# Optimization experiments

Hardware: AMD Instinct MI355X
Metric: run time of the kernel (lower is better)

The kernel has to match this reference:

```python
import jax, jax.numpy as jnp
import numpy as np


def _pairwise_iou(boxes):
    # boxes: [B, N, 4] in (x1, y1, x2, y2); returns IoU [B, N, N]
    area = (boxes[..., 2] - boxes[..., 0]) * (boxes[..., 3] - boxes[..., 1])  # [B, N]
    lt = jnp.maximum(boxes[:, :, None, :2], boxes[:, None, :, :2])  # [B, N, N, 2]
    rb = jnp.minimum(boxes[:, :, None, 2:], boxes[:, None, :, 2:])
    wh = jnp.clip(rb - lt, 0.0)
    inter = wh[..., 0] * wh[..., 1]  # [B, N, N]
    union = area[:, :, None] + area[:, None, :] - inter
    return inter / jnp.maximum(union, 1e-6)


def setup_inputs() -> dict:
    key = jax.random.key(0)
    kxy, kwh, ks = jax.random.split(key, 3)
    B, N, C = 4, 2048, 4
    xy = jax.random.uniform(kxy, (B, N, 2), dtype=jnp.float32) * 1000.0
    wh = jax.random.uniform(kwh, (B, N, 2), dtype=jnp.float32) * 100.0 + 1.0
    boxes = jnp.concatenate([xy, xy + wh], axis=-1)  # valid xyxy boxes
    scores = jax.random.uniform(ks, (B, C, N), dtype=jnp.float32)
    return {
        "boxes": boxes,
        "scores": scores,
        "iou_threshold": jnp.array([0.5], dtype=jnp.float32),
        "score_threshold": jnp.array([0.05], dtype=jnp.float32),
    }


def reference(boxes, scores, iou_threshold, score_threshold):
    # Greedy NMS-match (mmcv.ops.nms_match semantics), per batch and class.
    # Returns match: [B, C, N] int32 where match[b,c,n] is the index of the
    # group-leader (kept) box that box n belongs to, or -1 if unmatched
    # (i.e. score <= score_threshold).
    B, N, _ = boxes.shape
    C = scores.shape[1]
    thr = iou_threshold[0]
    sthr = score_threshold[0]

    iou = _pairwise_iou(boxes)  # [B, N, N] (shared across classes)
    order = jnp.argsort(-scores, axis=-1)  # [B, C, N], score-descending

    suppressed0 = scores <= sthr            # boxes below score threshold never match
    match0 = jnp.full((B, C, N), -1, jnp.int32)
    b_idx = jnp.arange(B)[:, None]          # [B, 1] for per-batch IoU row gather

    def step(carry, cand):
        # cand: [B, C] box index with next-highest score in each (batch, class)
        suppressed, match = carry           # [B, C, N] bool / int32
        cand_sup = jnp.take_along_axis(suppressed, cand[..., None], axis=-1)[..., 0]
        active = ~cand_sup                  # [B, C]: candidate not yet grouped
        cand_iou = iou[b_idx, cand]         # [B, C, N] IoU of candidate vs all boxes
        matched = active[..., None] & (~suppressed) & (cand_iou > thr)
        match = jnp.where(matched, cand[..., None].astype(jnp.int32), match)
        return (suppressed | matched, match), None

    xs = jnp.moveaxis(order, -1, 0)         # [N, B, C]: sequential greedy order
    (_, match), _ = jax.lax.scan(step, (suppressed0, match0), xs)
    return match
```

## Files before the change

kernel.cpp:

```cpp
#include <hip/hip_runtime.h>
#include <stdint.h>

#define N_   2048
#define NW   64
#define CLS  4
#define B_   4
#define ORD_STRIDE (N_ + 64)

__global__ __launch_bounds__(256) void mask_or_sort(
    const float4* __restrict__ boxes, const float* __restrict__ thr_p,
    const float* __restrict__ scores, const float* __restrict__ sthr_p,
    uint32_t* __restrict__ ov, int* __restrict__ order,
    int* __restrict__ rk, uint32_t* __restrict__ sup0ws)
{
  __shared__ __align__(16) unsigned char lds_raw[32768];
  __shared__ uint32_t sup_l[NW];
  __shared__ int cnt_s;

  if (blockIdx.x < 256) {
    float4* sb = (float4*)lds_raw;
    const int b    = blockIdx.x >> 6;
    const int tile = blockIdx.x & 63;
    const float thr = thr_p[0];
    for (int i = threadIdx.x; i < N_; i += 256) sb[i] = boxes[b * N_ + i];
    __syncthreads();
    const int wv = threadIdx.x >> 6;
    const int ln = threadIdx.x & 63;
    const int r0 = tile * 32 + wv * 8;
    float4 bi[8]; float areai[8];
    #pragma unroll
    for (int rr = 0; rr < 8; ++rr) {
      bi[rr] = sb[r0 + rr];
      areai[rr] = (bi[rr].z - bi[rr].x) * (bi[rr].w - bi[rr].y);
    }
    uint32_t myw[8] = {0, 0, 0, 0, 0, 0, 0, 0};
    for (int g = 0; g < 32; ++g) {
      const float4 bj = sb[g * 64 + ln];
      const float areaj = (bj.z - bj.x) * (bj.w - bj.y);
      const bool sel = ((ln >> 1) == g);
      const bool hi  = (ln & 1);
      #pragma unroll
      for (int rr = 0; rr < 8; ++rr) {
        const float xx1 = fmaxf(bi[rr].x, bj.x);
        const float yy1 = fmaxf(bi[rr].y, bj.y);
        const float xx2 = fminf(bi[rr].z, bj.z);
        const float yy2 = fminf(bi[rr].w, bj.w);
        const float iw = fmaxf(xx2 - xx1, 0.0f);
        const float ih = fmaxf(yy2 - yy1, 0.0f);
        const float inter = iw * ih;
        const float uni = fmaxf(areai[rr] + areaj - inter, 1e-6f);
        const unsigned long long bal = __ballot(inter / uni > thr);
        const uint32_t w = hi ? (uint32_t)(bal >> 32) : (uint32_t)bal;
        if (sel) myw[rr] = w;
      }
    }
    #pragma unroll
    for (int rr = 0; rr < 8; ++rr)
      ov[((size_t)(b * N_ + r0 + rr)) * NW + ln] = myw[rr];
  } else {
    unsigned long long* sp = (unsigned long long*)lds_raw;
    const int bc = blockIdx.x - 256;
    const float sthr = sthr_p[0];
    const float* s = scores + (size_t)bc * N_;
    for (int i = threadIdx.x; i < N_; i += 256) {
      const float v = s[i];
      uint32_t u = __float_as_uint(v);
      u = (u >> 31) ? ~u : (u | 0x80000000u);
      sp[i] = ((unsigned long long)u << 32) | (uint32_t)(~(uint32_t)i);
      const unsigned long long bal = __ballot(v <= sthr);
      if ((threadIdx.x & 63) == 0) {
        sup_l[(i >> 5)]     = (uint32_t)bal;
        sup_l[(i >> 5) + 1] = (uint32_t)(bal >> 32);
      }
    }
    for (int size = 2; size <= N_; size <<= 1) {
      for (int stride = size >> 1; stride > 0; stride >>= 1) {
        __syncthreads();
        for (int t = threadIdx.x; t < N_ / 2; t += 256) {
          const int pos = 2 * t - (t & (stride - 1));
          const bool desc = ((t & (size >> 1)) == 0);
          const unsigned long long a = sp[pos], c = sp[pos + stride];
          if (desc != (a > c)) { sp[pos] = c; sp[pos + stride] = a; }
        }
      }
    }
    __syncthreads();
    if (threadIdx.x == 0) {
      int c2 = 0;
      for (int w = 0; w < NW; ++w) c2 += __popc(sup_l[w]);
      cnt_s = N_ - c2;
    }
    __syncthreads();
    const int cnt = cnt_s;
    const int last = (cnt > 0) ? (int)~(uint32_t)sp[cnt - 1] : 0;
    int* ord_o = order + (size_t)bc * ORD_STRIDE;
    int* rk_o  = rk    + (size_t)bc * N_;
    for (int i = threadIdx.x; i < N_; i += 256) {
      const int idx = (int)~(uint32_t)sp[i];
      ord_o[i] = (i < cnt || cnt == 0) ? idx : last;
      rk_o[idx] = i;
    }
    for (int i = N_ + threadIdx.x; i < ORD_STRIDE; i += 256) ord_o[i] = last;
    if (threadIdx.x < NW) sup0ws[bc * NW + threadIdx.x] = sup_l[threadIdx.x];
  }
}


#define S6_(rw,bt) \
  "v_and_b32 v35, v" #rw ", v34\n\t"           \
  "v_cmp_ne_u32 vcc, 0, v35\n\t"               \
  "s_cmp_lg_u64 vcc, 0\n\t"                    \
  "s_cselect_b32 s40, 0, -1\n\t"               \
  "v_and_b32 v37, s40, v" #bt "\n\t"           \
  "v_or_b32 v34, v34, v37\n\t"

#define RF_(rw,st) \
  "v_lshlrev_b32 v38, 8, v" #st "\n\t"         \
  "v_add_u32 v38, v38, v33\n\t"                \
  "global_load_dword v" #rw ", v38, %[B]\n\t"

#define MB_(bt,st) \
  "v_bfe_u32 v36, v" #st ", 5, 6\n\t"          \
  "v_cmp_eq_u32 s[42:43], v36, v32\n\t"        \
  "v_cndmask_b32 v37, 0, v40, s[42:43]\n\t"    \
  "v_lshlrev_b32 v" #bt ", v" #st ", v37\n\t"

#define CAND(rw,bt,st) S6_(rw,bt) RF_(rw,st) MB_(bt,st)
#define CP(rw,bt,st)   RF_(rw,st) MB_(bt,st)

#define DSR4 \
  "ds_read_b128 v[140:143], v39\n\t"           \
  "ds_read_b128 v[144:147], v39 offset:16\n\t" \
  "ds_read_b128 v[148:151], v39 offset:32\n\t" \
  "ds_read_b128 v[152:155], v39 offset:48\n\t" \
  "v_add_u32 v39, 64, v39\n\t"

#define PH_HDR "s_waitcnt vmcnt(32)\n\t" "s_waitcnt lgkmcnt(0)\n\t"

#define PH_A PH_HDR \
  CAND(92,44,140)  CAND(93,45,141)  CAND(94,46,142)  CAND(95,47,143)  \
  CAND(96,48,144)  CAND(97,49,145)  CAND(98,50,146)  CAND(99,51,147)  \
  CAND(100,52,148) CAND(101,53,149) CAND(102,54,150) CAND(103,55,151) \
  CAND(104,56,152) CAND(105,57,153) CAND(106,58,154) CAND(107,59,155) DSR4
#define PH_B PH_HDR \
  CAND(108,60,140) CAND(109,61,141) CAND(110,62,142) CAND(111,63,143) \
  CAND(112,64,144) CAND(113,65,145) CAND(114,66,146) CAND(115,67,147) \
  CAND(116,68,148) CAND(117,69,149) CAND(118,70,150) CAND(119,71,151) \
  CAND(120,72,152) CAND(121,73,153) CAND(122,74,154) CAND(123,75,155) DSR4
#define PH_C PH_HDR \
  CAND(124,76,140) CAND(125,77,141) CAND(126,78,142) CAND(127,79,143) \
  CAND(128,80,144) CAND(129,81,145) CAND(130,82,146) CAND(131,83,147) \
  CAND(132,84,148) CAND(133,85,149) CAND(134,86,150) CAND(135,87,151) \
  CAND(136,88,152) CAND(137,89,153) CAND(138,90,154) CAND(139,91,155) DSR4

#define PRO_A \
  CP(92,44,140)  CP(93,45,141)  CP(94,46,142)  CP(95,47,143)  \
  CP(96,48,144)  CP(97,49,145)  CP(98,50,146)  CP(99,51,147)  \
  CP(100,52,148) CP(101,53,149) CP(102,54,150) CP(103,55,151) \
  CP(104,56,152) CP(105,57,153) CP(106,58,154) CP(107,59,155)
#define PRO_B \
  CP(108,60,140) CP(109,61,141) CP(110,62,142) CP(111,63,143) \
  CP(112,64,144) CP(113,65,145) CP(114,66,146) CP(115,67,147) \
  CP(116,68,148) CP(117,69,149) CP(118,70,150) CP(119,71,151) \
  CP(120,72,152) CP(121,73,153) CP(122,74,154) CP(123,75,155)
#define PRO_C \
  CP(124,76,140) CP(125,77,141) CP(126,78,142) CP(127,79,143) \
  CP(128,80,144) CP(129,81,145) CP(130,82,146) CP(131,83,147) \
  CP(132,84,148) CP(133,85,149) CP(134,86,150) CP(135,87,151) \
  CP(136,88,152) CP(137,89,153) CP(138,90,154) CP(139,91,155)

__global__ __launch_bounds__(256, 1) void scan_extract(
    const uint32_t* __restrict__ ov, const int* __restrict__ order,
    const int* __restrict__ rk, const uint32_t* __restrict__ sup0ws,
    int* __restrict__ match)
{
  __shared__ __align__(16) int sv[ORD_STRIDE];
  __shared__ __align__(16) int rk_s[N_];
  __shared__ uint32_t lead_s[NW];
  __shared__ uint32_t sup_s[NW];

  const int bc = blockIdx.x;
  const int b  = bc / CLS;

  {
    const int4* osrc = (const int4*)(order + (size_t)bc * ORD_STRIDE);
    int4* odst = (int4*)sv;
    for (int i = threadIdx.x; i < ORD_STRIDE / 4; i += 256) odst[i] = osrc[i];
    const int4* rsrc = (const int4*)(rk + (size_t)bc * N_);
    int4* rdst = (int4*)rk_s;
    for (int i = threadIdx.x; i < N_ / 4; i += 256) rdst[i] = rsrc[i];
    if (threadIdx.x < NW) sup_s[threadIdx.x] = sup0ws[bc * NW + threadIdx.x];
  }
  __syncthreads();

  if (threadIdx.x < 64) {
    const int l  = threadIdx.x;
    const int l4 = l << 2;
    const uint32_t cb = (uint32_t)(uintptr_t)(&sv[0]);
    const uint32_t* rowb = ov + (size_t)b * N_ * NW;
    uint32_t vlead;
    asm volatile(
      "s_waitcnt vmcnt(0) lgkmcnt(0)\n\t"
      "v_mov_b32 v32, %[LN]\n\t"
      "v_mov_b32 v33, %[L4]\n\t"
      "v_mov_b32 v34, 0\n\t"
      "v_mov_b32 v39, %[CB]\n\t"
      "v_mov_b32 v40, 1\n\t"
      DSR4 "s_waitcnt lgkmcnt(0)\n\t" PRO_A
      DSR4 "s_waitcnt lgkmcnt(0)\n\t" PRO_B
      DSR4 "s_waitcnt lgkmcnt(0)\n\t" PRO_C
      DSR4
      "s_mov_b32 s41, 42\n\t"
      "LSCAN%=:\n\t"
      PH_A PH_B PH_C
      "s_sub_u32 s41, s41, 1\n\t"
      "s_cmp_lg_u32 s41, 0\n\t"
      "s_cbranch_scc1 LSCAN%=\n\t"
      PH_A PH_B
      "s_waitcnt vmcnt(0) lgkmcnt(0)\n\t"
      "v_mov_b32 %[LD], v34\n\t"
      : [LD] "=v"(vlead)
      : [LN] "v"(l), [L4] "v"(l4), [CB] "v"(cb), [B] "s"(rowb)
      : "memory", "vcc", "scc", "s40", "s41", "s42", "s43",
        "v32","v33","v34","v35","v36","v37","v38","v39","v40","v41","v42","v43",
        "v44","v45","v46","v47","v48","v49","v50","v51","v52","v53","v54","v55",
        "v56","v57","v58","v59","v60","v61","v62","v63","v64","v65","v66","v67",
        "v68","v69","v70","v71","v72","v73","v74","v75","v76","v77","v78","v79",
        "v80","v81","v82","v83","v84","v85","v86","v87","v88","v89","v90","v91",
        "v92","v93","v94","v95","v96","v97","v98","v99","v100","v101","v102","v103",
        "v104","v105","v106","v107","v108","v109","v110","v111","v112","v113","v114","v115",
        "v116","v117","v118","v119","v120","v121","v122","v123","v124","v125","v126","v127",
        "v128","v129","v130","v131","v132","v133","v134","v135","v136","v137","v138","v139",
        "v140","v141","v142","v143","v144","v145","v146","v147","v148","v149","v150","v151",
        "v152","v153","v154","v155");
    lead_s[l] = vlead;
  }
  __syncthreads();

  const uint32_t* Mb = ov + (size_t)b * N_ * NW;
  for (int k = 0; k < 8; ++k) {
    const int n = (k << 8) + threadIdx.x;
    int res = -1;
    if (!((sup_s[n >> 5] >> (n & 31)) & 1u)) {
      const uint4* r4 = (const uint4*)(Mb + (size_t)n * NW);
      const uint4* g4 = (const uint4*)lead_s;
      int best = 1 << 30;
      #pragma unroll
      for (int j = 0; j < 16; ++j) {
        const uint4 a = r4[j];
        const uint4 g = g4[j];
        uint32_t w0 = a.x & g.x, w1 = a.y & g.y, w2 = a.z & g.z, w3 = a.w & g.w;
        while (w0) { const int bb = __ffs(w0) - 1; w0 &= w0 - 1;
          const int jj = (j << 7) + bb;      const int r = rk_s[jj];
          if (r < best) { best = r; res = jj; } }
        while (w1) { const int bb = __ffs(w1) - 1; w1 &= w1 - 1;
          const int jj = (j << 7) + 32 + bb; const int r = rk_s[jj];
          if (r < best) { best = r; res = jj; } }
        while (w2) { const int bb = __ffs(w2) - 1; w2 &= w2 - 1;
          const int jj = (j << 7) + 64 + bb; const int r = rk_s[jj];
          if (r < best) { best = r; res = jj; } }
        while (w3) { const int bb = __ffs(w3) - 1; w3 &= w3 - 1;
          const int jj = (j << 7) + 96 + bb; const int r = rk_s[jj];
          if (r < best) { best = r; res = jj; } }
      }
    }
    match[(size_t)bc * N_ + n] = res;
  }
}

extern "C" void kernel_launch(void* const* d_in, const int* in_sizes, int n_in,
                              void* d_out, int out_size, void* d_ws, size_t ws_size,
                              hipStream_t stream)
{
  const float4* boxes  = (const float4*)d_in[0];
  const float*  scores = (const float*)d_in[1];
  const float*  iouthr = (const float*)d_in[2];
  const float*  scthr  = (const float*)d_in[3];
  int* match = (int*)d_out;

  char* ws = (char*)d_ws;
  uint32_t* ov    = (uint32_t*)ws;
  int*      order = (int*)(ws + (size_t)B_ * N_ * NW * 4);
  int*      rk    = (int*)((char*)order + (size_t)B_ * CLS * ORD_STRIDE * 4);
  uint32_t* sup0  = (uint32_t*)((char*)rk + (size_t)B_ * CLS * N_ * 4);

  mask_or_sort<<<dim3(256 + B_ * CLS), dim3(256), 0, stream>>>(
      boxes, iouthr, scores, scthr, ov, order, rk, sup0);
  scan_extract<<<dim3(B_ * CLS), dim3(256), 0, stream>>>(
      ov, order, rk, sup0, match);
}
```

Measured before the change: 203.5 us.

## Split pipeline into four kernels and parallelize match extraction across 256 blocks

The fused mask/sort kernel is split into separate build_mask and sort_init launches. The serial leader scan becomes its own 64-thread kernel with a reworked asm schedule: independent instructions are interleaved with the loads, scalar-compare registers are used instead of VCC, and the last phases drain in order. Match extraction moves to a 256-block kernel where each wave handles one row, with a per-lane bit scan followed by a shuffle min-reduction. The goal is to stop the extraction phase running on only 16 blocks, at the cost of two extra launches and a workspace round-trip for the leader mask.

```diff
diff --git a/kernel.cpp b/kernel.cpp
--- a/kernel.cpp
+++ b/kernel.cpp
@@ -7,264 +7,309 @@
 #define B_   4
 #define ORD_STRIDE (N_ + 64)
 
-__global__ __launch_bounds__(256) void mask_or_sort(
+__global__ __launch_bounds__(256) void build_mask(
     const float4* __restrict__ boxes, const float* __restrict__ thr_p,
+    uint32_t* __restrict__ ov)
+{
+  __shared__ float4 sb[N_];
+  const int b    = blockIdx.x >> 6;
+  const int tile = blockIdx.x & 63;
+  const float thr = thr_p[0];
+  for (int i = threadIdx.x; i < N_; i += 256) sb[i] = boxes[b * N_ + i];
+  __syncthreads();
+  const int wv = threadIdx.x >> 6;
+  const int ln = threadIdx.x & 63;
+  const int r0 = tile * 32 + wv * 8;
+  float4 bi[8]; float areai[8];
+  #pragma unroll
+  for (int rr = 0; rr < 8; ++rr) {
+    bi[rr] = sb[r0 + rr];
+    areai[rr] = (bi[rr].z - bi[rr].x) * (bi[rr].w - bi[rr].y);
+  }
+  uint32_t myw[8] = {0, 0, 0, 0, 0, 0, 0, 0};
+  for (int g = 0; g < 32; ++g) {
+    const float4 bj = sb[g * 64 + ln];
+    const float areaj = (bj.z - bj.x) * (bj.w - bj.y);
+    const bool sel = ((ln >> 1) == g);
+    const bool hi  = (ln & 1);
+    #pragma unroll
+    for (int rr = 0; rr < 8; ++rr) {
+      const float xx1 = fmaxf(bi[rr].x, bj.x);
+      const float yy1 = fmaxf(bi[rr].y, bj.y);
+      const float xx2 = fminf(bi[rr].z, bj.z);
+      const float yy2 = fminf(bi[rr].w, bj.w);
+      const float iw = fmaxf(xx2 - xx1, 0.0f);
+      const float ih = fmaxf(yy2 - yy1, 0.0f);
+      const float inter = iw * ih;
+      const float uni = fmaxf(areai[rr] + areaj - inter, 1e-6f);
+      const unsigned long long bal = __ballot(inter / uni > thr);
+      const uint32_t w = hi ? (uint32_t)(bal >> 32) : (uint32_t)bal;
+      if (sel) myw[rr] = w;
+    }
+  }
+  #pragma unroll
+  for (int rr = 0; rr < 8; ++rr)
+    ov[((size_t)(b * N_ + r0 + rr)) * NW + ln] = myw[rr];
+}
+
+__global__ __launch_bounds__(256) void sort_init(
     const float* __restrict__ scores, const float* __restrict__ sthr_p,
-    uint32_t* __restrict__ ov, int* __restrict__ order,
-    int* __restrict__ rk, uint32_t* __restrict__ sup0ws)
-{
-  __shared__ __align__(16) unsigned char lds_raw[32768];
+    int* __restrict__ order, int* __restrict__ rk, uint32_t* __restrict__ sup0ws)
+{
+  __shared__ unsigned long long sp[N_];
   __shared__ uint32_t sup_l[NW];
   __shared__ int cnt_s;
-
-  if (blockIdx.x < 256) {
-    float4* sb = (float4*)lds_raw;
-    const int b    = blockIdx.x >> 6;
-    const int tile = blockIdx.x & 63;
-    const float thr = thr_p[0];
-    for (int i = threadIdx.x; i < N_; i += 256) sb[i] = boxes[b * N_ + i];
-    __syncthreads();
-    const int wv = threadIdx.x >> 6;
-    const int ln = threadIdx.x & 63;
-    const int r0 = tile * 32 + wv * 8;
-    float4 bi[8]; float areai[8];
-    #pragma unroll
-    for (int rr = 0; rr < 8; ++rr) {
-      bi[rr] = sb[r0 + rr];
-      areai[rr] = (bi[rr].z - bi[rr].x) * (bi[rr].w - bi[rr].y);
-    }
-    uint32_t myw[8] = {0, 0, 0, 0, 0, 0, 0, 0};
-    for (int g = 0; g < 32; ++g) {
-      const float4 bj = sb[g * 64 + ln];
-      const float areaj = (bj.z - bj.x) * (bj.w - bj.y);
-      const bool sel = ((ln >> 1) == g);
-      const bool hi  = (ln & 1);
-      #pragma unroll
-      for (int rr = 0; rr < 8; ++rr) {
-        const float xx1 = fmaxf(bi[rr].x, bj.x);
-        const float yy1 = fmaxf(bi[rr].y, bj.y);
-        const float xx2 = fminf(bi[rr].z, bj.z);
-        const float yy2 = fminf(bi[rr].w, bj.w);
-        const float iw = fmaxf(xx2 - xx1, 0.0f);
-        const float ih = fmaxf(yy2 - yy1, 0.0f);
-        const float inter = iw * ih;
-        const float uni = fmaxf(areai[rr] + areaj - inter, 1e-6f);
-        const unsigned long long bal = __ballot(inter / uni > thr);
-        const uint32_t w = hi ? (uint32_t)(bal >> 32) : (uint32_t)bal;
-        if (sel) myw[rr] = w;
+  const int bc = blockIdx.x;
+  const float sthr = sthr_p[0];
+  const float* s = scores + (size_t)bc * N_;
+  for (int i = threadIdx.x; i < N_; i += 256) {
+    const float v = s[i];
+    uint32_t u = __float_as_uint(v);
+    u = (u >> 31) ? ~u : (u | 0x80000000u);
+    sp[i] = ((unsigned long long)u << 32) | (uint32_t)(~(uint32_t)i);
+    const unsigned long long bal = __ballot(v <= sthr);
+    if ((threadIdx.x & 63) == 0) {
+      sup_l[(i >> 5)]     = (uint32_t)bal;
+      sup_l[(i >> 5) + 1] = (uint32_t)(bal >> 32);
+    }
+  }
+  for (int size = 2; size <= N_; size <<= 1) {
+    for (int stride = size >> 1; stride > 0; stride >>= 1) {
+      __syncthreads();
+      for (int t = threadIdx.x; t < N_ / 2; t += 256) {
+        const int pos = 2 * t - (t & (stride - 1));
+        const bool desc = ((t & (size >> 1)) == 0);
+        const unsigned long long a = sp[pos], c = sp[pos + stride];
+        if (desc != (a > c)) { sp[pos] = c; sp[pos + stride] = a; }
       }
     }
-    #pragma unroll
-    for (int rr = 0; rr < 8; ++rr)
-      ov[((size_t)(b * N_ + r0 + rr)) * NW + ln] = myw[rr];
-  } else {
-    unsigned long long* sp = (unsigned long long*)lds_raw;
-    const int bc = blockIdx.x - 256;
-    const float sthr = sthr_p[0];
-    const float* s = scores + (size_t)bc * N_;
-    for (int i = threadIdx.x; i < N_; i += 256) {
-      const float v = s[i];
-      uint32_t u = __float_as_uint(v);
-      u = (u >> 31) ? ~u : (u | 0x80000000u);
-      sp[i] = ((unsigned long long)u << 32) | (uint32_t)(~(uint32_t)i);
-      const unsigned long long bal = __ballot(v <= sthr);
-      if ((threadIdx.x & 63) == 0) {
-        sup_l[(i >> 5)]     = (uint32_t)bal;
-        sup_l[(i >> 5) + 1] = (uint32_t)(bal >> 32);
-      }
-    }
-    for (int size = 2; size <= N_; size <<= 1) {
-      for (int stride = size >> 1; stride > 0; stride >>= 1) {
-        __syncthreads();
-        for (int t = threadIdx.x; t < N_ / 2; t += 256) {
-          const int pos = 2 * t - (t & (stride - 1));
-          const bool desc = ((t & (size >> 1)) == 0);
-          const unsigned long long a = sp[pos], c = sp[pos + stride];
-          if (desc != (a > c)) { sp[pos] = c; sp[pos + stride] = a; }
-        }
-      }
-    }
-    __syncthreads();
-    if (threadIdx.x == 0) {
-      int c2 = 0;
-      for (int w = 0; w < NW; ++w) c2 += __popc(sup_l[w]);
-      cnt_s = N_ - c2;
-    }
-    __syncthreads();
-    const int cnt = cnt_s;
-    const int last = (cnt > 0) ? (int)~(uint32_t)sp[cnt - 1] : 0;
-    int* ord_o = order + (size_t)bc * ORD_STRIDE;
-    int* rk_o  = rk    + (size_t)bc * N_;
-    for (int i = threadIdx.x; i < N_; i += 256) {
-      const int idx = (int)~(uint32_t)sp[i];
-      ord_o[i] = (i < cnt || cnt == 0) ? idx : last;
-      rk_o[idx] = i;
-    }
-    for (int i = N_ + threadIdx.x; i < ORD_STRIDE; i += 256) ord_o[i] = last;
-    if (threadIdx.x < NW) sup0ws[bc * NW + threadIdx.x] = sup_l[threadIdx.x];
-  }
-}
-
-
-#define S6_(rw,bt) \
-  "v_and_b32 v35, v" #rw ", v34\n\t"           \
-  "v_cmp_ne_u32 vcc, 0, v35\n\t"               \
-  "s_cmp_lg_u64 vcc, 0\n\t"                    \
-  "s_cselect_b32 s40, 0, -1\n\t"               \
-  "v_and_b32 v37, s40, v" #bt "\n\t"           \
+  }
+  __syncthreads();
+  if (threadIdx.x == 0) {
+    int c2 = 0;
+    for (int w = 0; w < NW; ++w) c2 += __popc(sup_l[w]);
+    cnt_s = N_ - c2;
+  }
+  __syncthreads();
+  const int cnt = cnt_s;
+  const int last = (cnt > 0) ? (int)~(uint32_t)sp[cnt - 1] : 0;
+  int* ord_o = order + (size_t)bc * ORD_STRIDE;
+  int* rk_o  = rk    + (size_t)bc * N_;
+  for (int i = threadIdx.x; i < N_; i += 256) {
+    const int idx = (int)~(uint32_t)sp[i];
+    ord_o[i] = (i < cnt || cnt == 0) ? idx : last;
+    rk_o[idx] = i;
+  }
+  for (int i = N_ + threadIdx.x; i < ORD_STRIDE; i += 256) ord_o[i] = last;
+  if (threadIdx.x < NW) sup0ws[bc * NW + threadIdx.x] = sup_l[threadIdx.x];
+}
+
+
+#define C_(r,b,s) \
+  "v_and_b32 v36, v" #r ", v34\n\t"              \
+  "v_lshlrev_b32 v38, 8, v" #s "\n\t"            \
+  "v_cmp_ne_u32 s[46:47], 0, v36\n\t"            \
+  "v_add_u32 v38, v38, v33\n\t"                  \
+  "v_bfe_u32 v44, v" #s ", 5, 6\n\t"             \
+  "s_and_b64 s[46:47], s[46:47], s[46:47]\n\t"   \
+  "s_cselect_b32 s40, 0, -1\n\t"                 \
+  "global_load_dword v" #r ", v38, %[B]\n\t"     \
+  "v_and_b32 v37, s40, v" #b "\n\t"              \
+  "v_or_b32 v34, v34, v37\n\t"                   \
+  "v_cmp_eq_u32 s[48:49], v44, v32\n\t"          \
+  "v_cndmask_b32 v37, 0, v45, s[48:49]\n\t"      \
+  "v_lshlrev_b32 v" #b ", v" #s ", v37\n\t"
+
+#define P_(r,b,s) \
+  "v_lshlrev_b32 v38, 8, v" #s "\n\t"            \
+  "v_add_u32 v38, v38, v33\n\t"                  \
+  "global_load_dword v" #r ", v38, %[B]\n\t"     \
+  "v_bfe_u32 v44, v" #s ", 5, 6\n\t"             \
+  "v_cmp_eq_u32 s[48:49], v44, v32\n\t"          \
+  "v_cndmask_b32 v37, 0, v45, s[48:49]\n\t"      \
+  "v_lshlrev_b32 v" #b ", v" #s ", v37\n\t"
+
+#define E_(r,b) \
+  "v_and_b32 v36, v" #r ", v34\n\t"              \
+  "v_cmp_ne_u32 s[46:47], 0, v36\n\t"            \
+  "s_and_b64 s[46:47], s[46:47], s[46:47]\n\t"   \
+  "s_cselect_b32 s40, 0, -1\n\t"                 \
+  "v_and_b32 v37, s40, v" #b "\n\t"              \
   "v_or_b32 v34, v34, v37\n\t"
 
-#define RF_(rw,st) \
-  "v_lshlrev_b32 v38, 8, v" #st "\n\t"         \
-  "v_add_u32 v38, v38, v33\n\t"                \
-  "global_load_dword v" #rw ", v38, %[B]\n\t"
-
-#define MB_(bt,st) \
-  "v_bfe_u32 v36, v" #st ", 5, 6\n\t"          \
-  "v_cmp_eq_u32 s[42:43], v36, v32\n\t"        \
-  "v_cndmask_b32 v37, 0, v40, s[42:43]\n\t"    \
-  "v_lshlrev_b32 v" #bt ", v" #st ", v37\n\t"
-
-#define CAND(rw,bt,st) S6_(rw,bt) RF_(rw,st) MB_(bt,st)
-#define CP(rw,bt,st)   RF_(rw,st) MB_(bt,st)
-
-#define DSR4 \
-  "ds_read_b128 v[140:143], v39\n\t"           \
-  "ds_read_b128 v[144:147], v39 offset:16\n\t" \
-  "ds_read_b128 v[148:151], v39 offset:32\n\t" \
-  "ds_read_b128 v[152:155], v39 offset:48\n\t" \
+#define DSR0 \
+  "ds_read_b128 v[144:147], v39\n\t"             \
+  "ds_read_b128 v[148:151], v39 offset:16\n\t"   \
+  "ds_read_b128 v[152:155], v39 offset:32\n\t"   \
+  "ds_read_b128 v[156:159], v39 offset:48\n\t"   \
   "v_add_u32 v39, 64, v39\n\t"
-
-#define PH_HDR "s_waitcnt vmcnt(32)\n\t" "s_waitcnt lgkmcnt(0)\n\t"
-
-#define PH_A PH_HDR \
-  CAND(92,44,140)  CAND(93,45,141)  CAND(94,46,142)  CAND(95,47,143)  \
-  CAND(96,48,144)  CAND(97,49,145)  CAND(98,50,146)  CAND(99,51,147)  \
-  CAND(100,52,148) CAND(101,53,149) CAND(102,54,150) CAND(103,55,151) \
-  CAND(104,56,152) CAND(105,57,153) CAND(106,58,154) CAND(107,59,155) DSR4
-#define PH_B PH_HDR \
-  CAND(108,60,140) CAND(109,61,141) CAND(110,62,142) CAND(111,63,143) \
-  CAND(112,64,144) CAND(113,65,145) CAND(114,66,146) CAND(115,67,147) \
-  CAND(116,68,148) CAND(117,69,149) CAND(118,70,150) CAND(119,71,151) \
-  CAND(120,72,152) CAND(121,73,153) CAND(122,74,154) CAND(123,75,155) DSR4
-#define PH_C PH_HDR \
-  CAND(124,76,140) CAND(125,77,141) CAND(126,78,142) CAND(127,79,143) \
-  CAND(128,80,144) CAND(129,81,145) CAND(130,82,146) CAND(131,83,147) \
-  CAND(132,84,148) CAND(133,85,149) CAND(134,86,150) CAND(135,87,151) \
-  CAND(136,88,152) CAND(137,89,153) CAND(138,90,154) CAND(139,91,155) DSR4
-
-#define PRO_A \
-  CP(92,44,140)  CP(93,45,141)  CP(94,46,142)  CP(95,47,143)  \
-  CP(96,48,144)  CP(97,49,145)  CP(98,50,146)  CP(99,51,147)  \
-  CP(100,52,148) CP(101,53,149) CP(102,54,150) CP(103,55,151) \
-  CP(104,56,152) CP(105,57,153) CP(106,58,154) CP(107,59,155)
-#define PRO_B \
-  CP(108,60,140) CP(109,61,141) CP(110,62,142) CP(111,63,143) \
-  CP(112,64,144) CP(113,65,145) CP(114,66,146) CP(115,67,147) \
-  CP(116,68,148) CP(117,69,149) CP(118,70,150) CP(119,71,151) \
-  CP(120,72,152) CP(121,73,153) CP(122,74,154) CP(123,75,155)
-#define PRO_C \
-  CP(124,76,140) CP(125,77,141) CP(126,78,142) CP(127,79,143) \
-  CP(128,80,144) CP(129,81,145) CP(130,82,146) CP(131,83,147) \
-  CP(132,84,148) CP(133,85,149) CP(134,86,150) CP(135,87,151) \
-  CP(136,88,152) CP(137,89,153) CP(138,90,154) CP(139,91,155)
-
-__global__ __launch_bounds__(256, 1) void scan_extract(
-    const uint32_t* __restrict__ ov, const int* __restrict__ order,
-    const int* __restrict__ rk, const uint32_t* __restrict__ sup0ws,
+#define DSR1 \
+  "ds_read_b128 v[160:163], v39\n\t"             \
+  "ds_read_b128 v[164:167], v39 offset:16\n\t"   \
+  "ds_read_b128 v[168:171], v39 offset:32\n\t"   \
+  "ds_read_b128 v[172:175], v39 offset:48\n\t"   \
+  "v_add_u32 v39, 64, v39\n\t"
+#define DSR2 \
+  "ds_read_b128 v[176:179], v39\n\t"             \
+  "ds_read_b128 v[180:183], v39 offset:16\n\t"   \
+  "ds_read_b128 v[184:187], v39 offset:32\n\t"   \
+  "ds_read_b128 v[188:191], v39 offset:48\n\t"   \
+  "v_add_u32 v39, 64, v39\n\t"
+
+#define CL_A \
+  C_(96,48,144)  C_(97,49,145)  C_(98,50,146)  C_(99,51,147)  \
+  C_(100,52,148) C_(101,53,149) C_(102,54,150) C_(103,55,151) \
+  C_(104,56,152) C_(105,57,153) C_(106,58,154) C_(107,59,155) \
+  C_(108,60,156) C_(109,61,157) C_(110,62,158) C_(111,63,159)
+#define CL_B \
+  C_(112,64,160) C_(113,65,161) C_(114,66,162) C_(115,67,163) \
+  C_(116,68,164) C_(117,69,165) C_(118,70,166) C_(119,71,167) \
+  C_(120,72,168) C_(121,73,169) C_(122,74,170) C_(123,75,171) \
+  C_(124,76,172) C_(125,77,173) C_(126,78,174) C_(127,79,175)
+#define CL_C \
+  C_(128,80,176) C_(129,81,177) C_(130,82,178) C_(131,83,179) \
+  C_(132,84,180) C_(133,85,181) C_(134,86,182) C_(135,87,183) \
+  C_(136,88,184) C_(137,89,185) C_(138,90,186) C_(139,91,187) \
+  C_(140,92,188) C_(141,93,189) C_(142,94,190) C_(143,95,191)
+
+#define PL_A \
+  P_(96,48,144)  P_(97,49,145)  P_(98,50,146)  P_(99,51,147)  \
+  P_(100,52,148) P_(101,53,149) P_(102,54,150) P_(103,55,151) \
+  P_(104,56,152) P_(105,57,153) P_(106,58,154) P_(107,59,155) \
+  P_(108,60,156) P_(109,61,157) P_(110,62,158) P_(111,63,159)
+#define PL_B \
+  P_(112,64,160) P_(113,65,161) P_(114,66,162) P_(115,67,163) \
+  P_(116,68,164) P_(117,69,165) P_(118,70,166) P_(119,71,167) \
+  P_(120,72,168) P_(121,73,169) P_(122,74,170) P_(123,75,171) \
+  P_(124,76,172) P_(125,77,173) P_(126,78,174) P_(127,79,175)
+#define PL_C \
+  P_(128,80,176) P_(129,81,177) P_(130,82,178) P_(131,83,179) \
+  P_(132,84,180) P_(133,85,181) P_(134,86,182) P_(135,87,183) \
+  P_(136,88,184) P_(137,89,185) P_(138,90,186) P_(139,91,187) \
+  P_(140,92,188) P_(141,93,189) P_(142,94,190) P_(143,95,191)
+
+#define EL_A \
+  E_(96,48)  E_(97,49)  E_(98,50)  E_(99,51)  E_(100,52) E_(101,53) \
+  E_(102,54) E_(103,55) E_(104,56) E_(105,57) E_(106,58) E_(107,59) \
+  E_(108,60) E_(109,61) E_(110,62) E_(111,63)
+#define EL_B \
+  E_(112,64) E_(113,65) E_(114,66) E_(115,67) E_(116,68) E_(117,69) \
+  E_(118,70) E_(119,71) E_(120,72) E_(121,73) E_(122,74) E_(123,75) \
+  E_(124,76) E_(125,77) E_(126,78) E_(127,79)
+#define EL_C \
+  E_(128,80) E_(129,81) E_(130,82) E_(131,83) E_(132,84) E_(133,85) \
+  E_(134,86) E_(135,87) E_(136,88) E_(137,89) E_(138,90) E_(139,91) \
+  E_(140,92) E_(141,93) E_(142,94) E_(143,95)
+
+#define PH_A "s_waitcnt vmcnt(32)\n\t" "s_waitcnt lgkmcnt(0)\n\t" DSR1 CL_A
+#define PH_B "s_waitcnt vmcnt(32)\n\t" "s_waitcnt lgkmcnt(0)\n\t" DSR2 CL_B
+#define PH_C "s_waitcnt vmcnt(32)\n\t" "s_waitcnt lgkmcnt(0)\n\t" DSR0 CL_C
+
+__global__ __launch_bounds__(64, 1) void scan_lead(
+    const int* __restrict__ order, const uint32_t* __restrict__ ov,
+    uint32_t* __restrict__ leadws)
+{
+  __shared__ __align__(16) int sv[ORD_STRIDE];
+  const int bc = blockIdx.x;
+  const int b  = bc / CLS;
+  const int l  = threadIdx.x;
+  {
+    const int4* src = (const int4*)(order + (size_t)bc * ORD_STRIDE);
+    int4* dst = (int4*)sv;
+    for (int i = l; i < ORD_STRIDE / 4; i += 64) dst[i] = src[i];
+  }
+  const int l4 = l << 2;
+  const uint32_t cb = (uint32_t)(uintptr_t)(&sv[0]);
+  const uint32_t* rowb = ov + (size_t)b * N_ * NW;
+  uint32_t vlead;
+  asm volatile(
+    "s_waitcnt vmcnt(0) lgkmcnt(0)\n\t"
+    "v_mov_b32 v32, %[LN]\n\t"
+    "v_mov_b32 v33, %[L4]\n\t"
+    "v_mov_b32 v34, 0\n\t"
+    "v_mov_b32 v39, %[CB]\n\t"
+    "v_mov_b32 v45, 1\n\t"
+    DSR0 "s_waitcnt lgkmcnt(0)\n\t" PL_A
+    DSR1 "s_waitcnt lgkmcnt(0)\n\t" PL_B
+    DSR2 "s_waitcnt lgkmcnt(0)\n\t" PL_C
+    DSR0
+    "s_mov_b32 s41, 41\n\t"
+    "LSCAN%=:\n\t"
+    PH_A PH_B PH_C
+    "s_sub_u32 s41, s41, 1\n\t"
+    "s_cmp_lg_u32 s41, 0\n\t"
+    "s_cbranch_scc1 LSCAN%=\n\t"
+    PH_A PH_B
+    "s_waitcnt vmcnt(32)\n\t" EL_C
+    "s_waitcnt vmcnt(16)\n\t" EL_A
+    "s_waitcnt vmcnt(0)\n\t"  EL_B
+    "v_mov_b32 %[LD], v34\n\t"
+    : [LD] "=v"(vlead)
+    : [LN] "v"(l), [L4] "v"(l4), [CB] "v"(cb), [B] "s"(rowb)
+    : "memory", "scc", "s40", "s41", "s46", "s47", "s48", "s49",
+      "v32","v33","v34","v35","v36","v37","v38","v39","v44","v45",
+      "v48","v49","v50","v51","v52","v53","v54","v55",
+      "v56","v57","v58","v59","v60","v61","v62","v63","v64","v65","v66","v67",
+      "v68","v69","v70","v71","v72","v73","v74","v75","v76","v77","v78","v79",
+      "v80","v81","v82","v83","v84","v85","v86","v87","v88","v89","v90","v91",
+      "v92","v93","v94","v95","v96","v97","v98","v99","v100","v101","v102","v103",
+      "v104","v105","v106","v107","v108","v109","v110","v111","v112","v113","v114","v115",
+      "v116","v117","v118","v119","v120","v121","v122","v123","v124","v125","v126","v127",
+      "v128","v129","v130","v131","v132","v133","v134","v135","v136","v137","v138","v139",
+      "v140","v141","v142","v143","v144","v145","v146","v147","v148","v149","v150","v151",
+      "v152","v153","v154","v155","v156","v157","v158","v159","v160","v161","v162","v163",
+      "v164","v165","v166","v167","v168","v169","v170","v171","v172","v173","v174","v175",
+      "v176","v177","v178","v179","v180","v181","v182","v183","v184","v185","v186","v187",
+      "v188","v189","v190","v191");
+  leadws[bc * NW + l] = vlead;
+}
+
+__global__ __launch_bounds__(256) void extract_match(
+    const uint32_t* __restrict__ ov, const int* __restrict__ rk,
+    const uint32_t* __restrict__ sup0ws, const uint32_t* __restrict__ leadws,
     int* __restrict__ match)
 {
-  __shared__ __align__(16) int sv[ORD_STRIDE];
   __shared__ __align__(16) int rk_s[N_];
   __shared__ uint32_t lead_s[NW];
   __shared__ uint32_t sup_s[NW];
-
-  const int bc = blockIdx.x;
-  const int b  = bc / CLS;
-
+  const int bc  = blockIdx.x >> 4;
+  const int seg = blockIdx.x & 15;
+  const int b   = bc / CLS;
   {
-    const int4* osrc = (const int4*)(order + (size_t)bc * ORD_STRIDE);
-    int4* odst = (int4*)sv;
-    for (int i = threadIdx.x; i < ORD_STRIDE / 4; i += 256) odst[i] = osrc[i];
-    const int4* rsrc = (const int4*)(rk + (size_t)bc * N_);
-    int4* rdst = (int4*)rk_s;
-    for (int i = threadIdx.x; i < N_ / 4; i += 256) rdst[i] = rsrc[i];
-    if (threadIdx.x < NW) sup_s[threadIdx.x] = sup0ws[bc * NW + threadIdx.x];
+    const int4* src = (const int4*)(rk + (size_t)bc * N_);
+    int4* dst = (int4*)rk_s;
+    for (int i = threadIdx.x; i < N_ / 4; i += 256) dst[i] = src[i];
+    if (threadIdx.x < NW) {
+      lead_s[threadIdx.x] = leadws[bc * NW + threadIdx.x];
+      sup_s[threadIdx.x]  = sup0ws[bc * NW + threadIdx.x];
+    }
   }
   __syncthreads();
-
-  if (threadIdx.x < 64) {
-    const int l  = threadIdx.x;
-    const int l4 = l << 2;
-    const uint32_t cb = (uint32_t)(uintptr_t)(&sv[0]);
-    const uint32_t* rowb = ov + (size_t)b * N_ * NW;
-    uint32_t vlead;
-    asm volatile(
-      "s_waitcnt vmcnt(0) lgkmcnt(0)\n\t"
-      "v_mov_b32 v32, %[LN]\n\t"
-      "v_mov_b32 v33, %[L4]\n\t"
-      "v_mov_b32 v34, 0\n\t"
-      "v_mov_b32 v39, %[CB]\n\t"
-      "v_mov_b32 v40, 1\n\t"
-      DSR4 "s_waitcnt lgkmcnt(0)\n\t" PRO_A
-      DSR4 "s_waitcnt lgkmcnt(0)\n\t" PRO_B
-      DSR4 "s_waitcnt lgkmcnt(0)\n\t" PRO_C
-      DSR4
-      "s_mov_b32 s41, 42\n\t"
-      "LSCAN%=:\n\t"
-      PH_A PH_B PH_C
-      "s_sub_u32 s41, s41, 1\n\t"
-      "s_cmp_lg_u32 s41, 0\n\t"
-      "s_cbranch_scc1 LSCAN%=\n\t"
-      PH_A PH_B
-      "s_waitcnt vmcnt(0) lgkmcnt(0)\n\t"
-      "v_mov_b32 %[LD], v34\n\t"
-      : [LD] "=v"(vlead)
-      : [LN] "v"(l), [L4] "v"(l4), [CB] "v"(cb), [B] "s"(rowb)
-      : "memory", "vcc", "scc", "s40", "s41", "s42", "s43",
-        "v32","v33","v34","v35","v36","v37","v38","v39","v40","v41","v42","v43",
-        "v44","v45","v46","v47","v48","v49","v50","v51","v52","v53","v54","v55",
-        "v56","v57","v58","v59","v60","v61","v62","v63","v64","v65","v66","v67",
-        "v68","v69","v70","v71","v72","v73","v74","v75","v76","v77","v78","v79",
-        "v80","v81","v82","v83","v84","v85","v86","v87","v88","v89","v90","v91",
-        "v92","v93","v94","v95","v96","v97","v98","v99","v100","v101","v102","v103",
-        "v104","v105","v106","v107","v108","v109","v110","v111","v112","v113","v114","v115",
-        "v116","v117","v118","v119","v120","v121","v122","v123","v124","v125","v126","v127",
-        "v128","v129","v130","v131","v132","v133","v134","v135","v136","v137","v138","v139",
-        "v140","v141","v142","v143","v144","v145","v146","v147","v148","v149","v150","v151",
-        "v152","v153","v154","v155");
-    lead_s[l] = vlead;
-  }
-  __syncthreads();
-
+  const int wv = threadIdx.x >> 6;
+  const int l  = threadIdx.x & 63;
+  const uint32_t gl = lead_s[l];
   const uint32_t* Mb = ov + (size_t)b * N_ * NW;
-  for (int k = 0; k < 8; ++k) {
-    const int n = (k << 8) + threadIdx.x;
-    int res = -1;
-    if (!((sup_s[n >> 5] >> (n & 31)) & 1u)) {
-      const uint4* r4 = (const uint4*)(Mb + (size_t)n * NW);
-      const uint4* g4 = (const uint4*)lead_s;
-      int best = 1 << 30;
-      #pragma unroll
-      for (int j = 0; j < 16; ++j) {
-        const uint4 a = r4[j];
-        const uint4 g = g4[j];
-        uint32_t w0 = a.x & g.x, w1 = a.y & g.y, w2 = a.z & g.z, w3 = a.w & g.w;
-        while (w0) { const int bb = __ffs(w0) - 1; w0 &= w0 - 1;
-          const int jj = (j << 7) + bb;      const int r = rk_s[jj];
-          if (r < best) { best = r; res = jj; } }
-        while (w1) { const int bb = __ffs(w1) - 1; w1 &= w1 - 1;
-          const int jj = (j << 7) + 32 + bb; const int r = rk_s[jj];
-          if (r < best) { best = r; res = jj; } }
-        while (w2) { const int bb = __ffs(w2) - 1; w2 &= w2 - 1;
-          const int jj = (j << 7) + 64 + bb; const int r = rk_s[jj];
-          if (r < best) { best = r; res = jj; } }
-        while (w3) { const int bb = __ffs(w3) - 1; w3 &= w3 - 1;
-          const int jj = (j << 7) + 96 + bb; const int r = rk_s[jj];
-          if (r < best) { best = r; res = jj; } }
-      }
-    }
-    match[(size_t)bc * N_ + n] = res;
+  #pragma unroll 4
+  for (int j = 0; j < 32; ++j) {
+    const int n = seg * 128 + wv * 32 + j;
+    uint32_t bits = Mb[(size_t)n * NW + l] & gl;
+    int minp = 0x7FFFFFFF;
+    while (bits) {
+      const int k = __ffs(bits) - 1;
+      bits &= bits - 1;
+      const int jj = (l << 5) + k;
+      const int pk = (rk_s[jj] << 11) | jj;
+      minp = (pk < minp) ? pk : minp;
+    }
+    #pragma unroll
+    for (int m = 32; m; m >>= 1) {
+      const int o = __shfl_xor(minp, m);
+      minp = (o < minp) ? o : minp;
+    }
+    const bool below = (sup_s[n >> 5] >> (n & 31)) & 1u;
+    if (l == 0)
+      match[(size_t)bc * N_ + n] =
+          (below || minp == 0x7FFFFFFF) ? -1 : (minp & 2047);
   }
 }
 
@@ -283,9 +328,10 @@
   int*      order = (int*)(ws + (size_t)B_ * N_ * NW * 4);
   int*      rk    = (int*)((char*)order + (size_t)B_ * CLS * ORD_STRIDE * 4);
   uint32_t* sup0  = (uint32_t*)((char*)rk + (size_t)B_ * CLS * N_ * 4);
-
-  mask_or_sort<<<dim3(256 + B_ * CLS), dim3(256), 0, stream>>>(
-      boxes, iouthr, scores, scthr, ov, order, rk, sup0);
-  scan_extract<<<dim3(B_ * CLS), dim3(256), 0, stream>>>(
-      ov, order, rk, sup0, match);
-}
+  uint32_t* leadw = (uint32_t*)((char*)sup0 + (size_t)B_ * CLS * NW * 4);
+
+  build_mask   <<<dim3(256),      dim3(256), 0, stream>>>(boxes, iouthr, ov);
+  sort_init    <<<dim3(B_ * CLS), dim3(256), 0, stream>>>(scores, scthr, order, rk, sup0);
+  scan_lead    <<<dim3(B_ * CLS), dim3(64),  0, stream>>>(order, ov, leadw);
+  extract_match<<<dim3(256),      dim3(256), 0, stream>>>(ov, rk, sup0, leadw, match);
+}
```

New measurement: 196.0 us. 1.04x faster.
